# Optimization experiments

Measured on AMD Instinct MI355X. Metric: run time of the kernel, lower is better.

Reference implementation:

```python
import jax, jax.numpy as jnp
import numpy as np

BS = 8192      # total agents (batch)
T = 8          # trajectory length
NB = 128       # number of sub-batches (crowd groups)
BLK = BS // NB # agents per group = 64
EPS = 1e-7


def setup_inputs() -> dict:
    key = jax.random.key(0)
    ks = jax.random.split(key, 7)
    x = jax.random.normal(ks[0], (BS, T, 2), dtype=jnp.float32)
    # Kaiming-ish scaled params matching nn.Linear fan-in
    W1 = jax.random.normal(ks[1], (2, 32), dtype=jnp.float32) / np.sqrt(2.0)
    b1 = jax.random.normal(ks[2], (32,), dtype=jnp.float32) * 0.01
    W2 = jax.random.normal(ks[3], (32, 64), dtype=jnp.float32) / np.sqrt(32.0)
    b2 = jax.random.normal(ks[4], (64,), dtype=jnp.float32) * 0.01
    W3 = jax.random.normal(ks[5], (64, 64), dtype=jnp.float32) / np.sqrt(64.0)
    b3 = jax.random.normal(ks[6], (64,), dtype=jnp.float32) * 0.01
    starts = jnp.arange(NB, dtype=jnp.int32) * BLK
    sub_batches = jnp.stack([starts, starts + BLK], axis=1)  # [NB, 2]
    return {"x": x, "W1": W1, "b1": b1, "W2": W2, "b2": b2,
            "W3": W3, "b3": b3, "sub_batches": sub_batches}


def reference(x, W1, b1, W2, b2, W3, b3, sub_batches):
    bs = x.shape[0]
    xt = x[:, -1]                                   # [bs, 2] last timestep
    h = jax.nn.relu(xt @ W1 + b1)                   # [bs, 32]
    h = jax.nn.relu(h @ W2 + b2)                    # [bs, 64]
    h = h @ W3 + b3                                 # [bs, 64]

    nb = sub_batches.shape[0]
    blk = bs // nb
    hb = h.reshape(nb, blk, -1)                     # [nb, blk, 64]
    attn = jnp.einsum('nid,njd->nij', hb, hb)       # [nb, blk, blk]
    # Faithful to torch: attn - attn.max(1)[0] broadcasts row-max m[j]
    # along the LAST axis (attn[i,j] - m[j]).
    m = attn.max(axis=2)                            # [nb, blk]
    e = jnp.exp(attn - m[:, None, :])
    blocks = e / (e.sum(axis=2, keepdims=True) + EPS)

    # Scatter normalized blocks onto the block diagonal of a zero bs x bs matrix
    rows = sub_batches[:, 0][:, None] + jnp.arange(blk)  # [nb, blk]
    attens = jnp.zeros((bs, bs), dtype=h.dtype)
    attens = attens.at[rows[:, :, None], rows[:, None, :]].set(blocks)
    return attens
```

## Files before the change

### kernel.cpp

```cpp
#include <hip/hip_runtime.h>
#include <hip/hip_bf16.h>

#define BS   8192
#define TT   8
#define NB   128
#define BLK  64
#define EPS  1e-7f

__global__ __launch_bounds__(256) void attn_blocks(
    const float* __restrict__ x,
    const float* __restrict__ W1, const float* __restrict__ b1,
    const float* __restrict__ W2, const float* __restrict__ b2,
    const float* __restrict__ W3, const float* __restrict__ b3,
    const int*   __restrict__ sub_batches,
    float* __restrict__ out)
{
    __shared__ float sW1[2 * 32];
    __shared__ float sb1[32];
    __shared__ float sW2[32 * 64];
    __shared__ float sb2[64];
    __shared__ float sW3[64 * 64];
    __shared__ float sb3[64];
    __shared__ float h1[64][33];
    __shared__ float h2[64][65];
    __shared__ float h3[64][65];
    __shared__ float attn[64][65];
    __shared__ float mcol[64];
    __shared__ float rsum[64][4];

    const int tid = threadIdx.x;
    const int n   = blockIdx.x;
    const int start = sub_batches[2 * n];

    for (int i = tid; i < 2 * 32; i += 256)  sW1[i] = W1[i];
    if (tid < 32)                            sb1[tid] = b1[tid];
    for (int i = tid; i < 32 * 64; i += 256) sW2[i] = W2[i];
    if (tid < 64)                            sb2[tid] = b2[tid];
    for (int i = tid; i < 64 * 64; i += 256) sW3[i] = W3[i];
    if (tid >= 64 && tid < 128)              sb3[tid - 64] = b3[tid - 64];
    __syncthreads();

    const int row  = tid >> 2;
    const int part = tid & 3;

    const int r  = start + row;
    const float x0 = x[((long long)r * TT + (TT - 1)) * 2 + 0];
    const float x1 = x[((long long)r * TT + (TT - 1)) * 2 + 1];

    for (int f = part * 8; f < part * 8 + 8; ++f) {
        float v = fmaf(x0, sW1[f], fmaf(x1, sW1[32 + f], sb1[f]));
        h1[row][f] = v > 0.f ? v : 0.f;
    }
    __syncthreads();

    for (int f = part * 16; f < part * 16 + 16; ++f) {
        float acc = sb2[f];
        #pragma unroll
        for (int k = 0; k < 32; ++k) acc = fmaf(h1[row][k], sW2[k * 64 + f], acc);
        h2[row][f] = acc > 0.f ? acc : 0.f;
    }
    __syncthreads();

    for (int f = part * 16; f < part * 16 + 16; ++f) {
        float acc = sb3[f];
        #pragma unroll
        for (int k = 0; k < 64; ++k) acc = fmaf(h2[row][k], sW3[k * 64 + f], acc);
        h3[row][f] = acc;
    }
    __syncthreads();

    for (int j = part * 16; j < part * 16 + 16; ++j) {
        float acc = 0.f;
        #pragma unroll
        for (int k = 0; k < 64; ++k) acc = fmaf(h3[row][k], h3[j][k], acc);
        attn[row][j] = acc;
    }
    __syncthreads();

    if (tid < 64) {
        float mx = attn[tid][0];
        #pragma unroll
        for (int k = 1; k < 64; ++k) mx = fmaxf(mx, attn[tid][k]);
        mcol[tid] = mx;
    }
    __syncthreads();

    float ps = 0.f;
    for (int j = part * 16; j < part * 16 + 16; ++j) {
        float e = expf(attn[row][j] - mcol[j]);
        attn[row][j] = e;
        ps += e;
    }
    rsum[row][part] = ps;
    __syncthreads();

    const float s   = rsum[row][0] + rsum[row][1] + rsum[row][2] + rsum[row][3] + EPS;
    const float inv = 1.f / s;

    const long long base = (long long)(start + row) * BS + start;
    for (int j = part * 16; j < part * 16 + 16; ++j) {
        out[base + j] = attn[row][j] * inv;
    }
}

extern "C" void kernel_launch(void* const* d_in, const int* in_sizes, int n_in,
                              void* d_out, int out_size, void* d_ws, size_t ws_size,
                              hipStream_t stream) {
    const float* x   = (const float*)d_in[0];
    const float* W1  = (const float*)d_in[1];
    const float* b1  = (const float*)d_in[2];
    const float* W2  = (const float*)d_in[3];
    const float* b2  = (const float*)d_in[4];
    const float* W3  = (const float*)d_in[5];
    const float* b3  = (const float*)d_in[6];
    const int*   sb  = (const int*)d_in[7];
    float* out = (float*)d_out;

    hipMemsetAsync(out, 0, (size_t)BS * BS * sizeof(float), stream);

    attn_blocks<<<NB, 256, 0, stream>>>(x, W1, b1, W2, b2, W3, b3, sb, out);
}
```

Before: 296.0 us.

## Fuse zero-fill into attention kernel, skip diagonal blocks, vectorize LDS math

Drops the separate hipMemsetAsync over the whole 8192x8192 output. The zero fill now runs in extra thread blocks of the same launch, which write float4 zeros everywhere except the diagonal 64x64 blocks. The compute blocks also use float4 LDS reads and register accumulators for the MLP and attention dot products, reuse h2 as the attention buffer, and store results with float4 writes. This saves one launch and the redundant zeroing of diagonal blocks. In exchange it depends on the fixed contiguous sub_batches layout to know which regions to skip.

```diff
diff --git a/kernel.cpp b/kernel.cpp
--- a/kernel.cpp
+++ b/kernel.cpp
@@ -1,5 +1,4 @@
 #include <hip/hip_runtime.h>
-#include <hip/hip_bf16.h>
 
 #define BS   8192
 #define TT   8
@@ -7,7 +6,10 @@
 #define BLK  64
 #define EPS  1e-7f
 
-__global__ __launch_bounds__(256) void attn_blocks(
+#define FILL_ITERS 16
+#define NFILL      ((BS * (BS / 4)) / (256 * FILL_ITERS))
+
+__global__ __launch_bounds__(256, 2) void attn_fused(
     const float* __restrict__ x,
     const float* __restrict__ W1, const float* __restrict__ b1,
     const float* __restrict__ W2, const float* __restrict__ b2,
@@ -15,21 +17,36 @@
     const int*   __restrict__ sub_batches,
     float* __restrict__ out)
 {
+    const int tid = threadIdx.x;
+    const int bid = blockIdx.x;
+
+    if (bid >= NB) {
+        float4* __restrict__ out4 = (float4*)out;
+        const float4 z = make_float4(0.f, 0.f, 0.f, 0.f);
+        const int base = (bid - NB) * (256 * FILL_ITERS) + tid;
+        #pragma unroll
+        for (int it = 0; it < FILL_ITERS; ++it) {
+            const int idx  = base + it * 256;
+            const int row  = idx >> 11;
+            const int col4 = idx & 2047;
+            if ((col4 >> 4) != (row >> 6)) out4[idx] = z;
+        }
+        return;
+    }
+
+    __shared__ __align__(16) float sW2[32 * 64];
+    __shared__ __align__(16) float sW3[64 * 64];
+    __shared__ __align__(16) float h1[64][36];
+    __shared__ __align__(16) float h2[64][68];
+    __shared__ __align__(16) float h3[64][68];
     __shared__ float sW1[2 * 32];
     __shared__ float sb1[32];
-    __shared__ float sW2[32 * 64];
     __shared__ float sb2[64];
-    __shared__ float sW3[64 * 64];
     __shared__ float sb3[64];
-    __shared__ float h1[64][33];
-    __shared__ float h2[64][65];
-    __shared__ float h3[64][65];
-    __shared__ float attn[64][65];
     __shared__ float mcol[64];
     __shared__ float rsum[64][4];
 
-    const int tid = threadIdx.x;
-    const int n   = blockIdx.x;
+    const int n     = bid;
     const int start = sub_batches[2 * n];
 
     for (int i = tid; i < 2 * 32; i += 256)  sW1[i] = W1[i];
@@ -40,66 +57,130 @@
     if (tid >= 64 && tid < 128)              sb3[tid - 64] = b3[tid - 64];
     __syncthreads();
 
-    const int row  = tid >> 2;
-    const int part = tid & 3;
-
-    const int r  = start + row;
-    const float x0 = x[((long long)r * TT + (TT - 1)) * 2 + 0];
-    const float x1 = x[((long long)r * TT + (TT - 1)) * 2 + 1];
-
-    for (int f = part * 8; f < part * 8 + 8; ++f) {
-        float v = fmaf(x0, sW1[f], fmaf(x1, sW1[32 + f], sb1[f]));
-        h1[row][f] = v > 0.f ? v : 0.f;
-    }
-    __syncthreads();
-
-    for (int f = part * 16; f < part * 16 + 16; ++f) {
-        float acc = sb2[f];
-        #pragma unroll
-        for (int k = 0; k < 32; ++k) acc = fmaf(h1[row][k], sW2[k * 64 + f], acc);
-        h2[row][f] = acc > 0.f ? acc : 0.f;
-    }
-    __syncthreads();
-
-    for (int f = part * 16; f < part * 16 + 16; ++f) {
-        float acc = sb3[f];
-        #pragma unroll
-        for (int k = 0; k < 64; ++k) acc = fmaf(h2[row][k], sW3[k * 64 + f], acc);
-        h3[row][f] = acc;
-    }
-    __syncthreads();
-
-    for (int j = part * 16; j < part * 16 + 16; ++j) {
-        float acc = 0.f;
-        #pragma unroll
-        for (int k = 0; k < 64; ++k) acc = fmaf(h3[row][k], h3[j][k], acc);
-        attn[row][j] = acc;
+    const int row = tid >> 2;
+    const int f0  = (tid & 3) * 16;
+
+    const int r = start + row;
+    const float2 xv = *(const float2*)&x[((size_t)r * TT + (TT - 1)) * 2];
+
+    {
+        const int g0 = (tid & 3) * 8;
+        #pragma unroll
+        for (int f = 0; f < 8; ++f) {
+            float v = fmaf(xv.x, sW1[g0 + f], fmaf(xv.y, sW1[32 + g0 + f], sb1[g0 + f]));
+            h1[row][g0 + f] = fmaxf(v, 0.f);
+        }
+    }
+    __syncthreads();
+
+    {
+        float acc[16];
+        #pragma unroll
+        for (int i = 0; i < 16; ++i) acc[i] = sb2[f0 + i];
+        for (int k = 0; k < 32; ++k) {
+            const float hk = h1[row][k];
+            const float4* wp = (const float4*)&sW2[k * 64 + f0];
+            #pragma unroll
+            for (int c = 0; c < 4; ++c) {
+                const float4 w = wp[c];
+                acc[4*c+0] = fmaf(hk, w.x, acc[4*c+0]);
+                acc[4*c+1] = fmaf(hk, w.y, acc[4*c+1]);
+                acc[4*c+2] = fmaf(hk, w.z, acc[4*c+2]);
+                acc[4*c+3] = fmaf(hk, w.w, acc[4*c+3]);
+            }
+        }
+        #pragma unroll
+        for (int c = 0; c < 4; ++c) {
+            float4 v = make_float4(fmaxf(acc[4*c+0], 0.f), fmaxf(acc[4*c+1], 0.f),
+                                   fmaxf(acc[4*c+2], 0.f), fmaxf(acc[4*c+3], 0.f));
+            ((float4*)&h2[row][f0])[c] = v;
+        }
+    }
+    __syncthreads();
+
+    {
+        float acc[16];
+        #pragma unroll
+        for (int i = 0; i < 16; ++i) acc[i] = sb3[f0 + i];
+        for (int k = 0; k < 64; ++k) {
+            const float hk = h2[row][k];
+            const float4* wp = (const float4*)&sW3[k * 64 + f0];
+            #pragma unroll
+            for (int c = 0; c < 4; ++c) {
+                const float4 w = wp[c];
+                acc[4*c+0] = fmaf(hk, w.x, acc[4*c+0]);
+                acc[4*c+1] = fmaf(hk, w.y, acc[4*c+1]);
+                acc[4*c+2] = fmaf(hk, w.z, acc[4*c+2]);
+                acc[4*c+3] = fmaf(hk, w.w, acc[4*c+3]);
+            }
+        }
+        #pragma unroll
+        for (int c = 0; c < 4; ++c) {
+            ((float4*)&h3[row][f0])[c] =
+                make_float4(acc[4*c+0], acc[4*c+1], acc[4*c+2], acc[4*c+3]);
+        }
+    }
+    __syncthreads();
+
+    float (*attn)[68] = h2;
+    {
+        float4 rv[16];
+        const float4* rp = (const float4*)&h3[row][0];
+        #pragma unroll
+        for (int kk = 0; kk < 16; ++kk) rv[kk] = rp[kk];
+
+        #pragma unroll
+        for (int jj = 0; jj < 16; ++jj) {
+            const int j = f0 + jj;
+            const float4* vp = (const float4*)&h3[j][0];
+            float s0 = 0.f, s1 = 0.f, s2 = 0.f, s3 = 0.f;
+            #pragma unroll
+            for (int kk = 0; kk < 16; ++kk) {
+                const float4 v = vp[kk];
+                s0 = fmaf(rv[kk].x, v.x, s0);
+                s1 = fmaf(rv[kk].y, v.y, s1);
+                s2 = fmaf(rv[kk].z, v.z, s2);
+                s3 = fmaf(rv[kk].w, v.w, s3);
+            }
+            attn[row][j] = (s0 + s1) + (s2 + s3);
+        }
     }
     __syncthreads();
 
     if (tid < 64) {
-        float mx = attn[tid][0];
-        #pragma unroll
-        for (int k = 1; k < 64; ++k) mx = fmaxf(mx, attn[tid][k]);
-        mcol[tid] = mx;
-    }
-    __syncthreads();
-
-    float ps = 0.f;
-    for (int j = part * 16; j < part * 16 + 16; ++j) {
-        float e = expf(attn[row][j] - mcol[j]);
-        attn[row][j] = e;
-        ps += e;
-    }
-    rsum[row][part] = ps;
+        const float4* ap = (const float4*)&attn[tid][0];
+        float4 m4 = ap[0];
+        #pragma unroll
+        for (int kk = 1; kk < 16; ++kk) {
+            const float4 v = ap[kk];
+            m4.x = fmaxf(m4.x, v.x); m4.y = fmaxf(m4.y, v.y);
+            m4.z = fmaxf(m4.z, v.z); m4.w = fmaxf(m4.w, v.w);
+        }
+        mcol[tid] = fmaxf(fmaxf(m4.x, m4.y), fmaxf(m4.z, m4.w));
+    }
+    __syncthreads();
+
+    {
+        float ps = 0.f;
+        #pragma unroll
+        for (int jj = 0; jj < 16; ++jj) {
+            const int j = f0 + jj;
+            const float e = expf(attn[row][j] - mcol[j]);
+            attn[row][j] = e;
+            ps += e;
+        }
+        rsum[row][tid & 3] = ps;
+    }
     __syncthreads();
 
     const float s   = rsum[row][0] + rsum[row][1] + rsum[row][2] + rsum[row][3] + EPS;
     const float inv = 1.f / s;
 
-    const long long base = (long long)(start + row) * BS + start;
-    for (int j = part * 16; j < part * 16 + 16; ++j) {
-        out[base + j] = attn[row][j] * inv;
+    float4* ob = (float4*)(out + (size_t)(start + row) * BS + start + f0);
+    #pragma unroll
+    for (int c = 0; c < 4; ++c) {
+        const float4 e4 = ((const float4*)&attn[row][f0])[c];
+        ob[c] = make_float4(e4.x * inv, e4.y * inv, e4.z * inv, e4.w * inv);
     }
 }
 
@@ -116,7 +197,5 @@
     const int*   sb  = (const int*)d_in[7];
     float* out = (float*)d_out;
 
-    hipMemsetAsync(out, 0, (size_t)BS * BS * sizeof(float), stream);
-
-    attn_blocks<<<NB, 256, 0, stream>>>(x, W1, b1, W2, b2, W3, b3, sb, out);
+    attn_fused<<<NB + NFILL, 256, 0, stream>>>(x, W1, b1, W2, b2, W3, b3, sb, out);
 }
```

New measurement: 265.3 us. -10.4%, faster.
